# Optimization experiments

Hardware: AMD Instinct MI355X
Metric: run time of the kernel (lower is better)

The kernel has to match this reference:

```python
import jax, jax.numpy as jnp
import numpy as np
from jax import lax

KERNEL = 3
SAMPLING_RATE = 100.0
N_GRID = 201  # np.linspace(-1, 1, 201) sub-sample grid


def setup_inputs() -> dict:
    key = jax.random.key(0)
    nb, nc, nx, nt = 32, 3, 64, 4096
    xcorr = jax.random.normal(key, (nb, nc, nx, nt), dtype=jnp.float32)
    return {"xcorr": xcorr, "nlag": nt // 2}


def reference(xcorr, nlag):
    nt = xcorr.shape[-1]
    x = jnp.abs(xcorr)  # vabs=True

    # max_pool2d with (1, kernel=3), stride 1, padding (0, 1) -> SAME max over lag axis
    smax = lax.reduce_window(
        x, -jnp.inf, lax.max,
        window_dimensions=(1, 1, 1, KERNEL),
        window_strides=(1, 1, 1, 1),
        padding=[(0, 0), (0, 0), (0, 0), (KERNEL // 2, KERNEL // 2)],
    )
    keep = (smax == x).astype(x.dtype)

    # top-2 local maxima along lag axis (sorted descending, like torch.topk)
    topk_score, topk_idx = lax.top_k(x * keep, 2)
    s0 = topk_score[..., 0]
    s1 = topk_score[..., 1]
    weight = (0.1 + 3.0 * (s0 - s1)) * s0 ** 2
    i0 = topk_idx[..., 0]  # [nb, nc, nx]

    # --- sub-sample interpolation: 3-point spline == parabola through neighbors ---
    offsets = jnp.array([-1, 0, 1], dtype=i0.dtype)
    nbr_idx = jnp.clip(i0[..., None] + offsets, 0, nt - 1)      # [nb,nc,nx,3]
    y = jnp.take_along_axis(x, nbr_idx, axis=-1)                 # [nb,nc,nx,3]
    ym1, y0, yp1 = y[..., 0], y[..., 1], y[..., 2]
    a = 0.5 * (ym1 + yp1) - y0   # quadratic coeff
    b = 0.5 * (yp1 - ym1)        # linear coeff
    c = y0                       # constant

    xg = jnp.linspace(-1.0, 1.0, N_GRID, dtype=x.dtype)          # [201]
    yg = (a[..., None] * xg + b[..., None]) * xg + c[..., None]  # [nb,nc,nx,201]
    ii = jnp.argmax(yg, axis=-1)                                  # [nb,nc,nx]
    sub_shift = xg[ii]
    topk_idx_f = i0.astype(x.dtype) + sub_shift
    topk_score0 = jnp.take_along_axis(yg, ii[..., None], axis=-1)[..., 0]

    # pick the channel with the largest weight
    idx = jnp.argmax(weight, axis=1, keepdims=True)               # [nb,1,nx]
    max_cc = jnp.take_along_axis(topk_score0, idx, axis=1)
    w = jnp.take_along_axis(weight, idx, axis=1)
    shift_idx = jnp.take_along_axis(topk_idx_f, idx, axis=1) - jnp.asarray(nlag, x.dtype)
    shift_t = shift_idx / SAMPLING_RATE

    # stacked: [cc_max, cc_weight, cc_dt, cc_shift], each [nb,1,nx]
    return jnp.stack([max_cc, w, shift_t, shift_idx], axis=0)
```

## Files before the change

### kernel.cpp

```cpp
#include <hip/hip_runtime.h>
#include <math.h>

#define NB 32
#define NC 3
#define NX 64
#define NT 4096
#define NROWS (NB * NC * NX)

struct Quad { float4 a, b, c, d; };

__device__ __forceinline__ Quad load_row(const float* __restrict__ xr, int wid, int lane) {
    const float* base = xr + (size_t)(wid << 10) + (size_t)(lane << 2);
    Quad q;
    q.a = *reinterpret_cast<const float4*>(base);
    q.b = *reinterpret_cast<const float4*>(base + 256);
    q.c = *reinterpret_cast<const float4*>(base + 512);
    q.d = *reinterpret_cast<const float4*>(base + 768);
    return q;
}

__device__ __forceinline__ void proc4(float a0, float a1, float a2, float a3,
                                      float cl, float cr, int t4,
                                      float& v0, int& i0, float& v1)
{
    const float c0 = (a0 >= cl && a0 >= a1) ? a0 : 0.0f;
    const float c1 = (a1 >= a0 && a1 >= a2) ? a1 : 0.0f;
    const float c2 = (a2 >= a1 && a2 >= a3) ? a2 : 0.0f;
    const float c3 = (a3 >= a2 && a3 >= cr) ? a3 : 0.0f;
    bool g;
    g = c0 > v0; v1 = g ? v0 : fmaxf(v1, c0); v0 = fmaxf(v0, c0); i0 = g ? t4     : i0;
    g = c1 > v0; v1 = g ? v0 : fmaxf(v1, c1); v0 = fmaxf(v0, c1); i0 = g ? t4 + 1 : i0;
    g = c2 > v0; v1 = g ? v0 : fmaxf(v1, c2); v0 = fmaxf(v0, c2); i0 = g ? t4 + 2 : i0;
    g = c3 > v0; v1 = g ? v0 : fmaxf(v1, c3); v0 = fmaxf(v0, c3); i0 = g ? t4 + 3 : i0;
}

__device__ __forceinline__ void scan_row(Quad q, float lmf, float rmf,
                                         int wid, int lane,
                                         float& v0, int& i0, float& v1)
{
    const int base = (wid << 10) + (lane << 2);
    v0 = -1.0f; v1 = -1.0f; i0 = 0;

    const float a00 = fabsf(q.a.x), a01 = fabsf(q.a.y), a02 = fabsf(q.a.z), a03 = fabsf(q.a.w);
    const float a10 = fabsf(q.b.x), a11 = fabsf(q.b.y), a12 = fabsf(q.b.z), a13 = fabsf(q.b.w);
    const float a20 = fabsf(q.c.x), a21 = fabsf(q.c.y), a22 = fabsf(q.c.z), a23 = fabsf(q.c.w);
    const float a30 = fabsf(q.d.x), a31 = fabsf(q.d.y), a32 = fabsf(q.d.z), a33 = fabsf(q.d.w);

    float lm, rm, t;

    lm = __shfl_up(a03, 1);
    lm = (lane == 0) ? ((wid > 0) ? lmf : -INFINITY) : lm;
    rm = __shfl_down(a00, 1);
    t  = __shfl(a10, 0);
    rm = (lane == 63) ? t : rm;
    proc4(a00, a01, a02, a03, lm, rm, base, v0, i0, v1);

    lm = __shfl_up(a13, 1);
    t  = __shfl(a03, 63);
    lm = (lane == 0) ? t : lm;
    rm = __shfl_down(a10, 1);
    t  = __shfl(a20, 0);
    rm = (lane == 63) ? t : rm;
    proc4(a10, a11, a12, a13, lm, rm, base + 256, v0, i0, v1);

    lm = __shfl_up(a23, 1);
    t  = __shfl(a13, 63);
    lm = (lane == 0) ? t : lm;
    rm = __shfl_down(a20, 1);
    t  = __shfl(a30, 0);
    rm = (lane == 63) ? t : rm;
    proc4(a20, a21, a22, a23, lm, rm, base + 512, v0, i0, v1);

    lm = __shfl_up(a33, 1);
    t  = __shfl(a23, 63);
    lm = (lane == 0) ? t : lm;
    rm = __shfl_down(a30, 1);
    rm = (lane == 63) ? ((wid < 3) ? rmf : -INFINITY) : rm;
    proc4(a30, a31, a32, a33, lm, rm, base + 768, v0, i0, v1);

    #pragma unroll
    for (int off = 1; off < 64; off <<= 1) {
        const float ov0 = __shfl_xor(v0, off);
        const int   oi0 = __shfl_xor(i0, off);
        const float ov1 = __shfl_xor(v1, off);
        const bool big = (ov0 > v0) || (ov0 == v0 && oi0 < i0);
        const float loser = big ? v0 : ov0;
        v1 = fmaxf(fmaxf(v1, ov1), loser);
        v0 = big ? ov0 : v0;
        i0 = big ? oi0 : i0;
    }
}

__device__ __forceinline__ void merge4(const float sv0c[4], const int si0c[4],
                                       const float sv1c[4],
                                       float& m0, int& mi, float& m1)
{
    m0 = sv0c[0]; mi = si0c[0]; m1 = sv1c[0];
    #pragma unroll
    for (int w = 1; w < 4; ++w) {
        const float b0 = sv0c[w]; const int bi = si0c[w]; const float b1 = sv1c[w];
        const bool big = (b0 > m0) || (b0 == m0 && bi < mi);
        const float loser = big ? m0 : b0;
        m1 = fmaxf(fmaxf(m1, b1), loser);
        m0 = big ? b0 : m0;
        mi = big ? bi : mi;
    }
}

__global__ __launch_bounds__(256) void scan_rows_kernel(
    const float* __restrict__ xcorr,
    float* __restrict__ wsv0, int* __restrict__ wsi0, float* __restrict__ wsv1)
{
    __shared__ float sv0[4], sv1[4];
    __shared__ int   si0[4];

    const int row  = blockIdx.x;
    const int tid  = threadIdx.x;
    const int lane = tid & 63;
    const int wid  = tid >> 6;

    const float* __restrict__ xr = xcorr + (size_t)row * NT;

    Quad q = load_row(xr, wid, lane);
    const int liE = (wid > 0) ? (wid << 10) - 1    : 0;
    const int riE = (wid < 3) ? (wid << 10) + 1024 : NT - 1;
    const float lm = fabsf(xr[liE]);
    const float rm = fabsf(xr[riE]);

    float v0, v1; int i0;
    scan_row(q, lm, rm, wid, lane, v0, i0, v1);

    if (lane == 0) { sv0[wid] = v0; si0[wid] = i0; sv1[wid] = v1; }
    __syncthreads();

    if (tid == 0) {
        float m0, m1; int mi;
        merge4(sv0, si0, sv1, m0, mi, m1);
        wsv0[row] = m0;
        wsi0[row] = mi;
        wsv1[row] = m1;
    }
}

__global__ __launch_bounds__(256) void epilogue_kernel(
    const float* __restrict__ xcorr,
    const float* __restrict__ wsv0, const int* __restrict__ wsi0,
    const float* __restrict__ wsv1,
    const int*   __restrict__ nlag_p,
    float* __restrict__ out)
{
    const int g = blockIdx.x * 256 + threadIdx.x;
    if (g >= NB * NX) return;
    const int b = g >> 6;
    const int x = g & 63;

    const int r0 = (b * NC + 0) * NX + x;
    const int r1 = (b * NC + 1) * NX + x;
    const int r2 = (b * NC + 2) * NX + x;

    const float m00 = wsv0[r0], m10 = wsv1[r0]; const int p0 = wsi0[r0];
    const float m01 = wsv0[r1], m11 = wsv1[r1]; const int p1 = wsi0[r1];
    const float m02 = wsv0[r2], m12 = wsv1[r2]; const int p2 = wsi0[r2];

    const float w0 = (0.1f + 3.0f * (m00 - m10)) * (m00 * m00);
    const float w1 = (0.1f + 3.0f * (m01 - m11)) * (m01 * m01);
    const float w2 = (0.1f + 3.0f * (m02 - m12)) * (m02 * m02);

    const bool t1 = w1 > w0;
    float bw = t1 ? w1 : w0;
    float bs = t1 ? m01 : m00;
    int   bp = t1 ? p1 : p0;
    int   rs = t1 ? r1 : r0;
    const bool t2 = w2 > bw;
    bw = t2 ? w2 : bw;
    bs = t2 ? m02 : bs;
    bp = t2 ? p2 : bp;
    rs = t2 ? r2 : rs;

    const float* __restrict__ xrs = xcorr + (size_t)rs * NT;

    const float ym1 = fabsf(xrs[bp > 0 ? bp - 1 : 0]);
    const float yp1 = fabsf(xrs[bp < NT - 1 ? bp + 1 : NT - 1]);
    const float A = 0.5f * (ym1 + yp1) - bs;
    const float B = 0.5f * (yp1 - ym1);
    const float C = bs;

    int gi; float bv;
    if (A == 0.0f) {
        gi = (B > 0.0f) ? 200 : 0;
        const float xg = 0.01f * (float)(gi - 100);
        bv = (A * xg + B) * xg + C;
    } else {
        float gv = (1.0f - 0.5f * B / A) * 100.0f;
        gv = fminf(fmaxf(gv, 0.0f), 200.0f);
        const int glo = (int)gv;
        bv = -INFINITY; gi = 0;
        #pragma unroll
        for (int d = -1; d <= 2; ++d) {
            int gg = glo + d;
            gg = gg < 0 ? 0 : (gg > 200 ? 200 : gg);
            const float xg = 0.01f * (float)(gg - 100);
            const float yg = (A * xg + B) * xg + C;
            if (yg > bv) { bv = yg; gi = gg; }
        }
    }

    const float fidx = (float)bp + 0.01f * (float)(gi - 100);
    const float nlagf = (float)(*nlag_p);
    const float shift_idx = fidx - nlagf;
    const int n = NB * NX;
    out[0 * n + g] = bv;
    out[1 * n + g] = bw;
    out[2 * n + g] = shift_idx / 100.0f;
    out[3 * n + g] = shift_idx;
}

extern "C" void kernel_launch(void* const* d_in, const int* in_sizes, int n_in,
                              void* d_out, int out_size, void* d_ws, size_t ws_size,
                              hipStream_t stream) {
    const float* xcorr  = (const float*)d_in[0];
    const int*   nlag_p = (const int*)d_in[1];
    float* out = (float*)d_out;

    float* ws   = (float*)d_ws;
    float* wsv0 = ws;
    int*   wsi0 = (int*)(ws + NROWS);
    float* wsv1 = ws + 2 * NROWS;

    scan_rows_kernel<<<NROWS, 256, 0, stream>>>(xcorr, wsv0, wsi0, wsv1);

    epilogue_kernel<<<(NB * NX + 255) / 256, 256, 0, stream>>>(
        xcorr, wsv0, wsi0, wsv1, nlag_p, out);
}
```

Baseline: 24.69 us.

## Map one wavefront per row with software-pipelined chunk loads

Each wavefront now scans a whole 4096-element row in four 1024-element chunks, prefetching the next chunk while processing the current one, instead of splitting a row across four waves. This removes the shared-memory merge, the __syncthreads, and the separate scalar edge loads, and passes chunk boundary values through shuffles. The grid shrinks fourfold and each wave does more serial work with more registers live, which reduces memory-level parallelism per wave.

```diff
diff --git a/kernel.cpp b/kernel.cpp
--- a/kernel.cpp
+++ b/kernel.cpp
@@ -9,8 +9,9 @@
 
 struct Quad { float4 a, b, c, d; };
 
-__device__ __forceinline__ Quad load_row(const float* __restrict__ xr, int wid, int lane) {
-    const float* base = xr + (size_t)(wid << 10) + (size_t)(lane << 2);
+__device__ __forceinline__ Quad load_chunk(const float* __restrict__ xr,
+                                           int coff, int lane) {
+    const float* base = xr + (size_t)coff + (size_t)(lane << 2);
     Quad q;
     q.a = *reinterpret_cast<const float4*>(base);
     q.b = *reinterpret_cast<const float4*>(base + 256);
@@ -34,12 +35,11 @@
     g = c3 > v0; v1 = g ? v0 : fmaxf(v1, c3); v0 = fmaxf(v0, c3); i0 = g ? t4 + 3 : i0;
 }
 
-__device__ __forceinline__ void scan_row(Quad q, float lmf, float rmf,
-                                         int wid, int lane,
-                                         float& v0, int& i0, float& v1)
-{
-    const int base = (wid << 10) + (lane << 2);
-    v0 = -1.0f; v1 = -1.0f; i0 = 0;
+__device__ __forceinline__ void scan_chunk(Quad q, float lmf, float rmf,
+                                           int coff, int lane,
+                                           float& v0, int& i0, float& v1)
+{
+    const int base = coff + (lane << 2);
 
     const float a00 = fabsf(q.a.x), a01 = fabsf(q.a.y), a02 = fabsf(q.a.z), a03 = fabsf(q.a.w);
     const float a10 = fabsf(q.b.x), a11 = fabsf(q.b.y), a12 = fabsf(q.b.z), a13 = fabsf(q.b.w);
@@ -49,7 +49,7 @@
     float lm, rm, t;
 
     lm = __shfl_up(a03, 1);
-    lm = (lane == 0) ? ((wid > 0) ? lmf : -INFINITY) : lm;
+    lm = (lane == 0) ? lmf : lm;
     rm = __shfl_down(a00, 1);
     t  = __shfl(a10, 0);
     rm = (lane == 63) ? t : rm;
@@ -75,8 +75,42 @@
     t  = __shfl(a23, 63);
     lm = (lane == 0) ? t : lm;
     rm = __shfl_down(a30, 1);
-    rm = (lane == 63) ? ((wid < 3) ? rmf : -INFINITY) : rm;
+    rm = (lane == 63) ? rmf : rm;
     proc4(a30, a31, a32, a33, lm, rm, base + 768, v0, i0, v1);
+}
+
+__global__ __launch_bounds__(256) void scan_rows_kernel(
+    const float* __restrict__ xcorr,
+    float* __restrict__ wsv0, int* __restrict__ wsi0, float* __restrict__ wsv1)
+{
+    const int tid  = threadIdx.x;
+    const int lane = tid & 63;
+    const int wid  = tid >> 6;
+    const int row  = blockIdx.x * 4 + wid;
+
+    const float* __restrict__ xr = xcorr + (size_t)row * NT;
+
+    float v0 = -1.0f, v1 = -1.0f; int i0 = 0;
+    float pl, nf;
+
+    Quad qA = load_chunk(xr, 0, lane);
+    Quad qB = load_chunk(xr, 1024, lane);
+
+    nf = __shfl(fabsf(qB.a.x), 0);
+    scan_chunk(qA, -INFINITY, nf, 0, lane, v0, i0, v1);
+    pl = __shfl(fabsf(qA.d.w), 63);
+
+    qA = load_chunk(xr, 2048, lane);
+    nf = __shfl(fabsf(qA.a.x), 0);
+    scan_chunk(qB, pl, nf, 1024, lane, v0, i0, v1);
+    pl = __shfl(fabsf(qB.d.w), 63);
+
+    qB = load_chunk(xr, 3072, lane);
+    nf = __shfl(fabsf(qB.a.x), 0);
+    scan_chunk(qA, pl, nf, 2048, lane, v0, i0, v1);
+    pl = __shfl(fabsf(qA.d.w), 63);
+
+    scan_chunk(qB, pl, -INFINITY, 3072, lane, v0, i0, v1);
 
     #pragma unroll
     for (int off = 1; off < 64; off <<= 1) {
@@ -89,56 +123,11 @@
         v0 = big ? ov0 : v0;
         i0 = big ? oi0 : i0;
     }
-}
-
-__device__ __forceinline__ void merge4(const float sv0c[4], const int si0c[4],
-                                       const float sv1c[4],
-                                       float& m0, int& mi, float& m1)
-{
-    m0 = sv0c[0]; mi = si0c[0]; m1 = sv1c[0];
-    #pragma unroll
-    for (int w = 1; w < 4; ++w) {
-        const float b0 = sv0c[w]; const int bi = si0c[w]; const float b1 = sv1c[w];
-        const bool big = (b0 > m0) || (b0 == m0 && bi < mi);
-        const float loser = big ? m0 : b0;
-        m1 = fmaxf(fmaxf(m1, b1), loser);
-        m0 = big ? b0 : m0;
-        mi = big ? bi : mi;
-    }
-}
-
-__global__ __launch_bounds__(256) void scan_rows_kernel(
-    const float* __restrict__ xcorr,
-    float* __restrict__ wsv0, int* __restrict__ wsi0, float* __restrict__ wsv1)
-{
-    __shared__ float sv0[4], sv1[4];
-    __shared__ int   si0[4];
-
-    const int row  = blockIdx.x;
-    const int tid  = threadIdx.x;
-    const int lane = tid & 63;
-    const int wid  = tid >> 6;
-
-    const float* __restrict__ xr = xcorr + (size_t)row * NT;
-
-    Quad q = load_row(xr, wid, lane);
-    const int liE = (wid > 0) ? (wid << 10) - 1    : 0;
-    const int riE = (wid < 3) ? (wid << 10) + 1024 : NT - 1;
-    const float lm = fabsf(xr[liE]);
-    const float rm = fabsf(xr[riE]);
-
-    float v0, v1; int i0;
-    scan_row(q, lm, rm, wid, lane, v0, i0, v1);
-
-    if (lane == 0) { sv0[wid] = v0; si0[wid] = i0; sv1[wid] = v1; }
-    __syncthreads();
-
-    if (tid == 0) {
-        float m0, m1; int mi;
-        merge4(sv0, si0, sv1, m0, mi, m1);
-        wsv0[row] = m0;
-        wsi0[row] = mi;
-        wsv1[row] = m1;
+
+    if (lane == 0) {
+        wsv0[row] = v0;
+        wsi0[row] = i0;
+        wsv1[row] = v1;
     }
 }
 
@@ -227,7 +216,7 @@
     int*   wsi0 = (int*)(ws + NROWS);
     float* wsv1 = ws + 2 * NROWS;
 
-    scan_rows_kernel<<<NROWS, 256, 0, stream>>>(xcorr, wsv0, wsi0, wsv1);
+    scan_rows_kernel<<<NROWS / 4, 256, 0, stream>>>(xcorr, wsv0, wsi0, wsv1);
 
     epilogue_kernel<<<(NB * NX + 255) / 256, 256, 0, stream>>>(
         xcorr, wsv0, wsi0, wsv1, nlag_p, out);
```

After: 25.01 us. About the same (+1.3%).
